# Performance work log

Hardware: AMD Instinct MI355X
Metric: run time of the kernel (lower is better)

Reference implementation:

```python
import jax, jax.numpy as jnp
import numpy as np

S, B, H = 256, 64, 1024


def setup_inputs() -> dict:
    key = jax.random.key(0)
    ks = jax.random.split(key, 8)
    scale = 1.0 / np.sqrt(2 * H)  # nn.Linear default-ish scale
    return {
        "x": jax.random.normal(ks[0], (S, B, H), dtype=jnp.float32),
        "h0": jax.random.normal(ks[1], (B, H), dtype=jnp.float32),
        "c0": jax.random.normal(ks[2], (B, H), dtype=jnp.float32),
        "Wf": jax.random.normal(ks[3], (H, 2 * H), dtype=jnp.float32) * scale,
        "bf": jnp.zeros((H,), dtype=jnp.float32),
        "Wi": jax.random.normal(ks[4], (H, 2 * H), dtype=jnp.float32) * scale,
        "bi": jnp.zeros((H,), dtype=jnp.float32),
        "Wg": jax.random.normal(ks[5], (H, 2 * H), dtype=jnp.float32) * scale,
        "bg": jnp.zeros((H,), dtype=jnp.float32),
        "Wo": jax.random.normal(ks[6], (H, 2 * H), dtype=jnp.float32) * scale,
        "bo": jnp.zeros((H,), dtype=jnp.float32),
    }


def _lstm(x, h0, c0, Wf, bf, Wi, bi, Wg, bg, Wo, bo):
    nhid = h0.shape[-1]
    # Fuse the 4 gate Linears into one GEMM: W_all [4H, 2H], b_all [4H].
    W_all = jnp.concatenate([Wf, Wi, Wg, Wo], axis=0)
    b_all = jnp.concatenate([bf, bi, bg, bo], axis=0)
    Wx, Wh = W_all[:, :nhid], W_all[:, nhid:]  # x-part / h-part of cat([x,h])
    # Precompute input contribution for all timesteps: [S, B, 4H]
    xz = jnp.einsum("sbh,gh->sbg", x, Wx) + b_all

    def step(carry, xz_t):
        h, c = carry
        z = xz_t + h @ Wh.T  # [B, 4H]
        f, i, g, o = jnp.split(z, 4, axis=-1)
        f = jax.nn.sigmoid(f)
        i = jax.nn.sigmoid(i)
        g = jnp.tanh(g)
        o = jax.nn.sigmoid(o)
        c = f * c + i * g
        h = o * jnp.tanh(c)
        return (h, c), h

    (h_f, c_f), hseq = jax.lax.scan(step, (h0, c0), xz)
    return hseq, h_f, c_f


def reference(x, h0, c0, Wf, bf, Wi, bi, Wg, bg, Wo, bo):
    hseq, h_f, c_f = _lstm(x, h0, c0, Wf, bf, Wi, bi, Wg, bg, Wo, bo)
    # residual_con=False path in the original: return x + hidden_seq
    return x + hseq, h_f, c_f
```

## Files before the change

### kernel.cpp

```cpp
#include <hip/hip_runtime.h>

typedef __bf16 bf16x8 __attribute__((ext_vector_type(8)));
typedef float f32x4 __attribute__((ext_vector_type(4)));
typedef unsigned int u32x4 __attribute__((ext_vector_type(4)));

#define S_LEN 256
#define BATCH 64
#define HID   1024
#define NWG   256
#define SBH   (S_LEN * BATCH * HID)
#define BH    (BATCH * HID)
#define BAR_INTS 256

__device__ __forceinline__ float sigm(float v) { return 1.0f / (1.0f + __expf(-v)); }
__device__ __forceinline__ float tanh_fast(float v) {
  float e = __expf(-2.0f * __builtin_fabsf(v));
  float r = (1.0f - e) / (1.0f + e);
  return __builtin_copysignf(r, v);
}

__device__ __forceinline__ u32x4 cvt8(float4 a, float4 b) {
  union { unsigned short us[8]; u32x4 v; } r;
  r.us[0] = __builtin_bit_cast(unsigned short, (__bf16)a.x);
  r.us[1] = __builtin_bit_cast(unsigned short, (__bf16)a.y);
  r.us[2] = __builtin_bit_cast(unsigned short, (__bf16)a.z);
  r.us[3] = __builtin_bit_cast(unsigned short, (__bf16)a.w);
  r.us[4] = __builtin_bit_cast(unsigned short, (__bf16)b.x);
  r.us[5] = __builtin_bit_cast(unsigned short, (__bf16)b.y);
  r.us[6] = __builtin_bit_cast(unsigned short, (__bf16)b.z);
  r.us[7] = __builtin_bit_cast(unsigned short, (__bf16)b.w);
  return r.v;
}

#define LOAD16_X4(dst, base, MODS)                                            \
  asm volatile(                                                               \
      "global_load_dwordx4 %0,  %16, off offset:0 " MODS "\n\t"               \
      "global_load_dwordx4 %1,  %16, off offset:64 " MODS "\n\t"              \
      "global_load_dwordx4 %2,  %16, off offset:128 " MODS "\n\t"             \
      "global_load_dwordx4 %3,  %16, off offset:192 " MODS "\n\t"             \
      "global_load_dwordx4 %4,  %16, off offset:256 " MODS "\n\t"             \
      "global_load_dwordx4 %5,  %16, off offset:320 " MODS "\n\t"             \
      "global_load_dwordx4 %6,  %16, off offset:384 " MODS "\n\t"             \
      "global_load_dwordx4 %7,  %16, off offset:448 " MODS "\n\t"             \
      "global_load_dwordx4 %8,  %16, off offset:512 " MODS "\n\t"             \
      "global_load_dwordx4 %9,  %16, off offset:576 " MODS "\n\t"             \
      "global_load_dwordx4 %10, %16, off offset:640 " MODS "\n\t"             \
      "global_load_dwordx4 %11, %16, off offset:704 " MODS "\n\t"             \
      "global_load_dwordx4 %12, %16, off offset:768 " MODS "\n\t"             \
      "global_load_dwordx4 %13, %16, off offset:832 " MODS "\n\t"             \
      "global_load_dwordx4 %14, %16, off offset:896 " MODS "\n\t"             \
      "global_load_dwordx4 %15, %16, off offset:960 " MODS "\n\t"             \
      "s_waitcnt vmcnt(0)"                                                    \
      : "=&v"((dst)[0]), "=&v"((dst)[1]), "=&v"((dst)[2]), "=&v"((dst)[3]),   \
        "=&v"((dst)[4]), "=&v"((dst)[5]), "=&v"((dst)[6]), "=&v"((dst)[7]),   \
        "=&v"((dst)[8]), "=&v"((dst)[9]), "=&v"((dst)[10]), "=&v"((dst)[11]), \
        "=&v"((dst)[12]), "=&v"((dst)[13]), "=&v"((dst)[14]), "=&v"((dst)[15])\
      : "v"(base)                                                             \
      : "memory")

__global__ void prep_kernel(const float* __restrict__ x, const float* __restrict__ h0,
                            const float* __restrict__ Wf, const float* __restrict__ Wi,
                            const float* __restrict__ Wg, const float* __restrict__ Wo,
                            __bf16* __restrict__ x_bf, __bf16* __restrict__ w_x,
                            __bf16* __restrict__ w_h, __bf16* __restrict__ h_buf,
                            int* __restrict__ bar) {
  size_t tid = (size_t)blockIdx.x * blockDim.x + threadIdx.x;
  size_t stride = (size_t)gridDim.x * blockDim.x;

  for (size_t i = tid; i < (size_t)(SBH / 8); i += stride) {
    const float4* s = (const float4*)x + i * 2;
    ((u32x4*)x_bf)[i] = cvt8(s[0], s[1]);
  }

#define W_CONV(W, gidx)                                                        \
  for (size_t i = tid; i < (size_t)(1024 * 128); i += stride) {                \
    int j   = (int)(i >> 7);                                                   \
    int kc8 = (int)(i & 127);                                                  \
    const float* row = (W) + (size_t)j * 2048;                                 \
    const float4* sx = (const float4*)(row + kc8 * 8);                         \
    const float4* sh = (const float4*)(row + 1024 + kc8 * 8);                  \
    size_t dst = (size_t)((gidx) * 1024 + j) * 128 + kc8;                      \
    ((u32x4*)w_x)[dst] = cvt8(sx[0], sx[1]);                                   \
    ((u32x4*)w_h)[dst] = cvt8(sh[0], sh[1]);                                   \
  }
  W_CONV(Wf, 0)
  W_CONV(Wi, 1)
  W_CONV(Wg, 2)
  W_CONV(Wo, 3)
#undef W_CONV

  for (size_t i = tid; i < (size_t)(BH / 8); i += stride) {
    const float4* s = (const float4*)h0 + i * 2;
    ((u32x4*)h_buf)[i] = cvt8(s[0], s[1]);
  }

  for (size_t i = tid; i < BAR_INTS; i += stride) bar[i] = 0;
}

__global__ __launch_bounds__(256, 1) void lstm_kernel(
    const float* __restrict__ x, const float* __restrict__ c0,
    const float* __restrict__ bfp, const float* __restrict__ bip,
    const float* __restrict__ bgp, const float* __restrict__ bop,
    const __bf16* __restrict__ x_bf, const __bf16* __restrict__ w_x,
    const __bf16* __restrict__ w_h, __bf16* __restrict__ h_buf,
    int* __restrict__ bar, float* __restrict__ out) {
  const int tid    = threadIdx.x;
  const int wgid   = blockIdx.x;
  const int m_idx  = wgid & 3;
  const int m_base = m_idx * 16;
  const int U      = (wgid >> 2) * 16;
  const int wave   = tid >> 6;
  const int lane   = tid & 63;
  const int l16    = lane & 15;
  const int kq8    = (lane >> 4) * 8;
  const int wg_in_grp = wgid >> 2;

  int* slots   = bar + m_idx * 64;

  __shared__ float zbuf[4][16][65];

  u32x4 Braw[64];
  {
    const __bf16* wsrc = (wave < 2) ? w_h : w_x;
    const int kbase = (wave & 1) * 512;
#pragma unroll
    for (int n = 0; n < 4; ++n) {
      unsigned long gb =
          (unsigned long)(wsrc + (size_t)(n * 1024 + U + l16) * HID + kbase + kq8);
      LOAD16_X4(&Braw[n * 16], gb, "");
    }
  }

  const int b_loc  = tid >> 4;
  const int u_loc  = tid & 15;
  const int j_t    = U + u_loc;
  const int b_glob = m_base + b_loc;
  float c = c0[(size_t)b_glob * HID + j_t];
  const float bias_f = bfp[j_t], bias_i = bip[j_t], bias_g = bgp[j_t], bias_o = bop[j_t];

  u32x4 Araw[16];
  if (wave >= 2) {
    const __bf16* xp =
        x_bf + ((size_t)(0 * BATCH + m_base + l16)) * HID + (wave & 1) * 512 + kq8;
#pragma unroll
    for (int kc = 0; kc < 16; ++kc) Araw[kc] = *(const u32x4*)(xp + kc * 32);
  }

  for (int t = 0; t < S_LEN; ++t) {
    const size_t roff = (t & 1) ? (size_t)BH : 0;
    const size_t woff = (t & 1) ? 0 : (size_t)BH;

    if (wave < 2) {
      unsigned long ga = (unsigned long)(h_buf + roff + (size_t)(m_base + l16) * HID +
                                         (wave & 1) * 512 + kq8);
      LOAD16_X4(Araw, ga, "sc0 sc1");
    }

    f32x4 acc0 = {0,0,0,0}, acc1 = {0,0,0,0}, acc2 = {0,0,0,0}, acc3 = {0,0,0,0};
#pragma unroll
    for (int kc = 0; kc < 16; ++kc) {
      bf16x8 a = __builtin_bit_cast(bf16x8, Araw[kc]);
      acc0 = __builtin_amdgcn_mfma_f32_16x16x32_bf16(a, __builtin_bit_cast(bf16x8, Braw[ 0 + kc]), acc0, 0, 0, 0);
      acc1 = __builtin_amdgcn_mfma_f32_16x16x32_bf16(a, __builtin_bit_cast(bf16x8, Braw[16 + kc]), acc1, 0, 0, 0);
      acc2 = __builtin_amdgcn_mfma_f32_16x16x32_bf16(a, __builtin_bit_cast(bf16x8, Braw[32 + kc]), acc2, 0, 0, 0);
      acc3 = __builtin_amdgcn_mfma_f32_16x16x32_bf16(a, __builtin_bit_cast(bf16x8, Braw[48 + kc]), acc3, 0, 0, 0);
    }

    {
      int q = lane >> 4;
#pragma unroll
      for (int r = 0; r < 4; ++r) {
        zbuf[wave][q * 4 + r][ 0 + l16] = acc0[r];
        zbuf[wave][q * 4 + r][16 + l16] = acc1[r];
        zbuf[wave][q * 4 + r][32 + l16] = acc2[r];
        zbuf[wave][q * 4 + r][48 + l16] = acc3[r];
      }
    }
    __syncthreads();

    float h;
    {
      float zf = 0.f, zi = 0.f, zg = 0.f, zo = 0.f;
#pragma unroll
      for (int w = 0; w < 4; ++w) {
        zf += zbuf[w][b_loc][ 0 + u_loc];
        zi += zbuf[w][b_loc][16 + u_loc];
        zg += zbuf[w][b_loc][32 + u_loc];
        zo += zbuf[w][b_loc][48 + u_loc];
      }
      float fg = sigm(zf + bias_f);
      float ig = sigm(zi + bias_i);
      float gg = tanh_fast(zg + bias_g);
      float og = sigm(zo + bias_o);
      c = fg * c + ig * gg;
      h = og * tanh_fast(c);
      if (t < S_LEN - 1) {
        __bf16 hb16 = (__bf16)h;
        unsigned short hbits = __builtin_bit_cast(unsigned short, hb16);
        __hip_atomic_store((unsigned short*)(h_buf + woff + (size_t)b_glob * HID + j_t),
                           hbits, __ATOMIC_RELAXED, __HIP_MEMORY_SCOPE_AGENT);
      }
    }

    if (t < S_LEN - 1) {
      __syncthreads();
      if (tid == 0) {
        __hip_atomic_store(&slots[wg_in_grp], t + 1,
                           __ATOMIC_RELAXED, __HIP_MEMORY_SCOPE_AGENT);
      }
      {
        size_t oi = ((size_t)(t * BATCH + b_glob)) * HID + j_t;
        out[oi] = x[oi] + h;
      }
      if (wave >= 2) {
        const __bf16* xp = x_bf +
            ((size_t)((t + 1) * BATCH + m_base + l16)) * HID + (wave & 1) * 512 + kq8;
#pragma unroll
        for (int kc = 0; kc < 16; ++kc) Araw[kc] = *(const u32x4*)(xp + kc * 32);
      }
      if (wave == 0) {
        const int target = t + 1;
        while (true) {
          int v = __hip_atomic_load(&slots[lane],
                                    __ATOMIC_RELAXED, __HIP_MEMORY_SCOPE_AGENT);
          if (__ballot(v >= target) == ~0ull) break;
          __builtin_amdgcn_s_sleep(1);
        }
      }
      __syncthreads();
    } else {
      size_t oi = ((size_t)(t * BATCH + b_glob)) * HID + j_t;
      out[oi] = x[oi] + h;
      out[(size_t)SBH + (size_t)b_glob * HID + j_t] = h;
      out[(size_t)SBH + BH + (size_t)b_glob * HID + j_t] = c;
    }
  }
}

extern "C" void kernel_launch(void* const* d_in, const int* in_sizes, int n_in,
                              void* d_out, int out_size, void* d_ws, size_t ws_size,
                              hipStream_t stream) {
  const float* x   = (const float*)d_in[0];
  const float* h0  = (const float*)d_in[1];
  const float* c0  = (const float*)d_in[2];
  const float* Wf  = (const float*)d_in[3];
  const float* bf_ = (const float*)d_in[4];
  const float* Wi  = (const float*)d_in[5];
  const float* bi_ = (const float*)d_in[6];
  const float* Wg  = (const float*)d_in[7];
  const float* bg_ = (const float*)d_in[8];
  const float* Wo  = (const float*)d_in[9];
  const float* bo_ = (const float*)d_in[10];

  char* ws = (char*)d_ws;
  size_t off = 0;
  __bf16* x_bf = (__bf16*)(ws + off); off += (size_t)SBH * 2;
  __bf16* w_x  = (__bf16*)(ws + off); off += (size_t)4 * 1024 * 1024 * 2;
  __bf16* w_h  = (__bf16*)(ws + off); off += (size_t)4 * 1024 * 1024 * 2;
  __bf16* h_buf = (__bf16*)(ws + off); off += (size_t)2 * BH * 2;
  int* bar = (int*)(ws + off); off += BAR_INTS * sizeof(int);
  if (ws_size < off) return;

  float* out = (float*)d_out;

  prep_kernel<<<2048, 256, 0, stream>>>(x, h0, Wf, Wi, Wg, Wo, x_bf, w_x, w_h, h_buf, bar);
  lstm_kernel<<<NWG, 256, 0, stream>>>(x, c0, bf_, bi_, bg_, bo_, x_bf, w_x, w_h, h_buf, bar, out);
}
```

Baseline: 1.149 ms.

## Overlap next-step x-projection MFMAs with barrier wait, pack h stores

Each wave now owns a 256-wide K slice of both Wh and Wx instead of splitting waves between the h and x parts. The x-part MFMAs for step t+1 are computed during the inter-workgroup barrier wait of step t, so each step's critical path only runs the h-part GEMM. The h output is staged in shared memory and written with 32 vectorized 16-byte stores instead of 256 scalar atomic stores. The spin-wait moves to wave 1, and the x operand for step t+2 is prefetched one step ahead.

```diff
diff --git a/kernel.cpp b/kernel.cpp
--- a/kernel.cpp
+++ b/kernel.cpp
@@ -32,29 +32,19 @@
   return r.v;
 }
 
-#define LOAD16_X4(dst, base, MODS)                                            \
+#define LOAD8_X4(dst, base, MODS)                                             \
   asm volatile(                                                               \
-      "global_load_dwordx4 %0,  %16, off offset:0 " MODS "\n\t"               \
-      "global_load_dwordx4 %1,  %16, off offset:64 " MODS "\n\t"              \
-      "global_load_dwordx4 %2,  %16, off offset:128 " MODS "\n\t"             \
-      "global_load_dwordx4 %3,  %16, off offset:192 " MODS "\n\t"             \
-      "global_load_dwordx4 %4,  %16, off offset:256 " MODS "\n\t"             \
-      "global_load_dwordx4 %5,  %16, off offset:320 " MODS "\n\t"             \
-      "global_load_dwordx4 %6,  %16, off offset:384 " MODS "\n\t"             \
-      "global_load_dwordx4 %7,  %16, off offset:448 " MODS "\n\t"             \
-      "global_load_dwordx4 %8,  %16, off offset:512 " MODS "\n\t"             \
-      "global_load_dwordx4 %9,  %16, off offset:576 " MODS "\n\t"             \
-      "global_load_dwordx4 %10, %16, off offset:640 " MODS "\n\t"             \
-      "global_load_dwordx4 %11, %16, off offset:704 " MODS "\n\t"             \
-      "global_load_dwordx4 %12, %16, off offset:768 " MODS "\n\t"             \
-      "global_load_dwordx4 %13, %16, off offset:832 " MODS "\n\t"             \
-      "global_load_dwordx4 %14, %16, off offset:896 " MODS "\n\t"             \
-      "global_load_dwordx4 %15, %16, off offset:960 " MODS "\n\t"             \
+      "global_load_dwordx4 %0, %8, off offset:0 " MODS "\n\t"                 \
+      "global_load_dwordx4 %1, %8, off offset:64 " MODS "\n\t"                \
+      "global_load_dwordx4 %2, %8, off offset:128 " MODS "\n\t"               \
+      "global_load_dwordx4 %3, %8, off offset:192 " MODS "\n\t"               \
+      "global_load_dwordx4 %4, %8, off offset:256 " MODS "\n\t"               \
+      "global_load_dwordx4 %5, %8, off offset:320 " MODS "\n\t"               \
+      "global_load_dwordx4 %6, %8, off offset:384 " MODS "\n\t"               \
+      "global_load_dwordx4 %7, %8, off offset:448 " MODS "\n\t"               \
       "s_waitcnt vmcnt(0)"                                                    \
       : "=&v"((dst)[0]), "=&v"((dst)[1]), "=&v"((dst)[2]), "=&v"((dst)[3]),   \
-        "=&v"((dst)[4]), "=&v"((dst)[5]), "=&v"((dst)[6]), "=&v"((dst)[7]),   \
-        "=&v"((dst)[8]), "=&v"((dst)[9]), "=&v"((dst)[10]), "=&v"((dst)[11]), \
-        "=&v"((dst)[12]), "=&v"((dst)[13]), "=&v"((dst)[14]), "=&v"((dst)[15])\
+        "=&v"((dst)[4]), "=&v"((dst)[5]), "=&v"((dst)[6]), "=&v"((dst)[7])    \
       : "v"(base)                                                             \
       : "memory")
 
@@ -113,22 +103,26 @@
   const int lane   = tid & 63;
   const int l16    = lane & 15;
   const int kq8    = (lane >> 4) * 8;
+  const int kbase  = wave * 256;
   const int wg_in_grp = wgid >> 2;
 
-  int* slots   = bar + m_idx * 64;
+  int* slots = bar + m_idx * 64;
 
   __shared__ float zbuf[4][16][65];
+  __shared__ __bf16 hpack[16][16];
 
   u32x4 Braw[64];
-  {
-    const __bf16* wsrc = (wave < 2) ? w_h : w_x;
-    const int kbase = (wave & 1) * 512;
-#pragma unroll
-    for (int n = 0; n < 4; ++n) {
-      unsigned long gb =
-          (unsigned long)(wsrc + (size_t)(n * 1024 + U + l16) * HID + kbase + kq8);
-      LOAD16_X4(&Braw[n * 16], gb, "");
-    }
+#pragma unroll
+  for (int n = 0; n < 4; ++n) {
+    unsigned long gbh =
+        (unsigned long)(w_h + (size_t)(n * 1024 + U + l16) * HID + kbase + kq8);
+    LOAD8_X4(&Braw[n * 8], gbh, "");
+  }
+#pragma unroll
+  for (int n = 0; n < 4; ++n) {
+    unsigned long gbx =
+        (unsigned long)(w_x + (size_t)(n * 1024 + U + l16) * HID + kbase + kq8);
+    LOAD8_X4(&Braw[32 + n * 8], gbx, "");
   }
 
   const int b_loc  = tid >> 4;
@@ -138,32 +132,46 @@
   float c = c0[(size_t)b_glob * HID + j_t];
   const float bias_f = bfp[j_t], bias_i = bip[j_t], bias_g = bgp[j_t], bias_o = bop[j_t];
 
-  u32x4 Araw[16];
-  if (wave >= 2) {
-    const __bf16* xp =
-        x_bf + ((size_t)(0 * BATCH + m_base + l16)) * HID + (wave & 1) * 512 + kq8;
-#pragma unroll
-    for (int kc = 0; kc < 16; ++kc) Araw[kc] = *(const u32x4*)(xp + kc * 32);
+  u32x4 Araw_x[8];
+  {
+    const __bf16* xp = x_bf + (size_t)(m_base + l16) * HID + kbase + kq8;
+#pragma unroll
+    for (int kc = 0; kc < 8; ++kc) Araw_x[kc] = *(const u32x4*)(xp + kc * 32);
+  }
+  f32x4 accx0 = {0,0,0,0}, accx1 = {0,0,0,0}, accx2 = {0,0,0,0}, accx3 = {0,0,0,0};
+#pragma unroll
+  for (int kc = 0; kc < 8; ++kc) {
+    bf16x8 a = __builtin_bit_cast(bf16x8, Araw_x[kc]);
+    accx0 = __builtin_amdgcn_mfma_f32_16x16x32_bf16(a, __builtin_bit_cast(bf16x8, Braw[32 +  0 + kc]), accx0, 0, 0, 0);
+    accx1 = __builtin_amdgcn_mfma_f32_16x16x32_bf16(a, __builtin_bit_cast(bf16x8, Braw[32 +  8 + kc]), accx1, 0, 0, 0);
+    accx2 = __builtin_amdgcn_mfma_f32_16x16x32_bf16(a, __builtin_bit_cast(bf16x8, Braw[32 + 16 + kc]), accx2, 0, 0, 0);
+    accx3 = __builtin_amdgcn_mfma_f32_16x16x32_bf16(a, __builtin_bit_cast(bf16x8, Braw[32 + 24 + kc]), accx3, 0, 0, 0);
+  }
+  {
+    const __bf16* xp = x_bf + (size_t)(BATCH + m_base + l16) * HID + kbase + kq8;
+#pragma unroll
+    for (int kc = 0; kc < 8; ++kc) Araw_x[kc] = *(const u32x4*)(xp + kc * 32);
   }
 
   for (int t = 0; t < S_LEN; ++t) {
     const size_t roff = (t & 1) ? (size_t)BH : 0;
     const size_t woff = (t & 1) ? 0 : (size_t)BH;
 
-    if (wave < 2) {
+    u32x4 Araw_h[8];
+    {
       unsigned long ga = (unsigned long)(h_buf + roff + (size_t)(m_base + l16) * HID +
-                                         (wave & 1) * 512 + kq8);
-      LOAD16_X4(Araw, ga, "sc0 sc1");
-    }
-
-    f32x4 acc0 = {0,0,0,0}, acc1 = {0,0,0,0}, acc2 = {0,0,0,0}, acc3 = {0,0,0,0};
-#pragma unroll
-    for (int kc = 0; kc < 16; ++kc) {
-      bf16x8 a = __builtin_bit_cast(bf16x8, Araw[kc]);
+                                         kbase + kq8);
+      LOAD8_X4(Araw_h, ga, "sc0 sc1");
+    }
+
+    f32x4 acc0 = accx0, acc1 = accx1, acc2 = accx2, acc3 = accx3;
+#pragma unroll
+    for (int kc = 0; kc < 8; ++kc) {
+      bf16x8 a = __builtin_bit_cast(bf16x8, Araw_h[kc]);
       acc0 = __builtin_amdgcn_mfma_f32_16x16x32_bf16(a, __builtin_bit_cast(bf16x8, Braw[ 0 + kc]), acc0, 0, 0, 0);
-      acc1 = __builtin_amdgcn_mfma_f32_16x16x32_bf16(a, __builtin_bit_cast(bf16x8, Braw[16 + kc]), acc1, 0, 0, 0);
-      acc2 = __builtin_amdgcn_mfma_f32_16x16x32_bf16(a, __builtin_bit_cast(bf16x8, Braw[32 + kc]), acc2, 0, 0, 0);
-      acc3 = __builtin_amdgcn_mfma_f32_16x16x32_bf16(a, __builtin_bit_cast(bf16x8, Braw[48 + kc]), acc3, 0, 0, 0);
+      acc1 = __builtin_amdgcn_mfma_f32_16x16x32_bf16(a, __builtin_bit_cast(bf16x8, Braw[ 8 + kc]), acc1, 0, 0, 0);
+      acc2 = __builtin_amdgcn_mfma_f32_16x16x32_bf16(a, __builtin_bit_cast(bf16x8, Braw[16 + kc]), acc2, 0, 0, 0);
+      acc3 = __builtin_amdgcn_mfma_f32_16x16x32_bf16(a, __builtin_bit_cast(bf16x8, Braw[24 + kc]), acc3, 0, 0, 0);
     }
 
     {
@@ -194,31 +202,49 @@
       float og = sigm(zo + bias_o);
       c = fg * c + ig * gg;
       h = og * tanh_fast(c);
-      if (t < S_LEN - 1) {
-        __bf16 hb16 = (__bf16)h;
-        unsigned short hbits = __builtin_bit_cast(unsigned short, hb16);
-        __hip_atomic_store((unsigned short*)(h_buf + woff + (size_t)b_glob * HID + j_t),
-                           hbits, __ATOMIC_RELAXED, __HIP_MEMORY_SCOPE_AGENT);
-      }
     }
 
     if (t < S_LEN - 1) {
+      hpack[b_loc][u_loc] = (__bf16)h;
       __syncthreads();
+
+      if (tid < 32) {
+        int b = tid >> 1, hf = tid & 1;
+        u32x4 hv = *(const u32x4*)(&hpack[b][hf * 8]);
+        unsigned long ha = (unsigned long)(h_buf + woff +
+                                           (size_t)(m_base + b) * HID + U + hf * 8);
+        asm volatile("global_store_dwordx4 %0, %1, off sc0 sc1\n\t"
+                     "s_waitcnt vmcnt(0)"
+                     :: "v"(ha), "v"(hv) : "memory");
+      }
       if (tid == 0) {
         __hip_atomic_store(&slots[wg_in_grp], t + 1,
                            __ATOMIC_RELAXED, __HIP_MEMORY_SCOPE_AGENT);
       }
+
       {
         size_t oi = ((size_t)(t * BATCH + b_glob)) * HID + j_t;
         out[oi] = x[oi] + h;
       }
-      if (wave >= 2) {
-        const __bf16* xp = x_bf +
-            ((size_t)((t + 1) * BATCH + m_base + l16)) * HID + (wave & 1) * 512 + kq8;
-#pragma unroll
-        for (int kc = 0; kc < 16; ++kc) Araw[kc] = *(const u32x4*)(xp + kc * 32);
-      }
-      if (wave == 0) {
+      accx0 = (f32x4){0,0,0,0}; accx1 = (f32x4){0,0,0,0};
+      accx2 = (f32x4){0,0,0,0}; accx3 = (f32x4){0,0,0,0};
+#pragma unroll
+      for (int kc = 0; kc < 8; ++kc) {
+        bf16x8 a = __builtin_bit_cast(bf16x8, Araw_x[kc]);
+        accx0 = __builtin_amdgcn_mfma_f32_16x16x32_bf16(a, __builtin_bit_cast(bf16x8, Braw[32 +  0 + kc]), accx0, 0, 0, 0);
+        accx1 = __builtin_amdgcn_mfma_f32_16x16x32_bf16(a, __builtin_bit_cast(bf16x8, Braw[32 +  8 + kc]), accx1, 0, 0, 0);
+        accx2 = __builtin_amdgcn_mfma_f32_16x16x32_bf16(a, __builtin_bit_cast(bf16x8, Braw[32 + 16 + kc]), accx2, 0, 0, 0);
+        accx3 = __builtin_amdgcn_mfma_f32_16x16x32_bf16(a, __builtin_bit_cast(bf16x8, Braw[32 + 24 + kc]), accx3, 0, 0, 0);
+      }
+      {
+        int tn = (t + 2 < S_LEN) ? (t + 2) : (S_LEN - 1);
+        const __bf16* xp =
+            x_bf + ((size_t)(tn * BATCH + m_base + l16)) * HID + kbase + kq8;
+#pragma unroll
+        for (int kc = 0; kc < 8; ++kc) Araw_x[kc] = *(const u32x4*)(xp + kc * 32);
+      }
+
+      if (wave == 1) {
         const int target = t + 1;
         while (true) {
           int v = __hip_atomic_load(&slots[lane],
```

New measurement: 1.207 ms. 5.1% more time.
